# Kernel optimization log

Hardware: AMD Instinct MI355X
Metric: run time of the kernel (lower is better)

## Reference

```python
import jax, jax.numpy as jnp
import numpy as np

N, F_DIM, H_DIM = 8192, 128, 128

def setup_inputs() -> dict:
    key = jax.random.key(0)
    ks = jax.random.split(key, 7)
    inp = {
        "input": jax.random.normal(ks[0], (N, F_DIM), dtype=jnp.float32),
        "wavelets": jax.random.normal(ks[1], (N, N), dtype=jnp.float32) / np.sqrt(N),
        "wavelets_inv": jax.random.normal(ks[2], (N, N), dtype=jnp.float32) / np.sqrt(N),
        # layer 1 params
        "W1": jax.random.uniform(ks[3], (F_DIM, H_DIM), dtype=jnp.float32,
                                 minval=-np.sqrt(6.0/(F_DIM+H_DIM)), maxval=np.sqrt(6.0/(F_DIM+H_DIM))),
        "f1": jax.random.uniform(ks[4], (N,), dtype=jnp.float32, minval=0.9, maxval=1.1),
        # layer 2 params
        "W2": jax.random.uniform(ks[5], (H_DIM, H_DIM), dtype=jnp.float32,
                                 minval=-np.sqrt(6.0/(H_DIM+H_DIM)), maxval=np.sqrt(6.0/(H_DIM+H_DIM))),
        "f2": jax.random.uniform(ks[6], (N,), dtype=jnp.float32, minval=0.9, maxval=1.1),
    }
    return inp

def _gwnn_layer(features, wavelets, wavelets_inv, W, filt):
    # torch: wavelets @ diag(filt) @ (wavelets_inv @ (features @ W))
    # diag(filt) matmul == column-wise scale of wavelets (broadcast elementwise)
    xw = features @ W                      # [N, out]
    spec = wavelets_inv @ xw               # [N, out] spectral-domain features
    spec = filt[:, None] * spec            # apply learnable diagonal filter
    return wavelets @ spec                 # [N, out]

def reference(input, wavelets, wavelets_inv, W1, f1, W2, f2):
    # eval mode: dropout is identity
    h1 = jax.nn.relu(_gwnn_layer(input, wavelets, wavelets_inv, W1, f1))
    out = _gwnn_layer(h1, wavelets, wavelets_inv, W2, f2)
    return out
```

## Files before the change

kernel.cpp:

```cpp
#include <hip/hip_runtime.h>
#include <hip/hip_bf16.h>
#include <stdint.h>


typedef __attribute__((ext_vector_type(4))) float f32x4;
typedef __attribute__((ext_vector_type(8))) short s16x8;
typedef __attribute__((ext_vector_type(4))) short s16x4;

#define DEVI static __device__ __forceinline__

DEVI short bf1(float x){ __bf16 h = (__bf16)x; return __builtin_bit_cast(short, h); }

DEVI s16x8 cvt8(f32x4 lo, f32x4 hi){
  s16x8 r;
#pragma unroll
  for (int i = 0; i < 4; ++i){ r[i] = bf1(lo[i]); r[4+i] = bf1(hi[i]); }
  return r;
}

DEVI void glds16(const void* g, void* l){
  __builtin_amdgcn_global_load_lds((const __attribute__((address_space(1))) void*)g,
                                   (__attribute__((address_space(3))) void*)l, 16, 0, 0);
}

template<int N> DEVI void waitvm(){
  if constexpr (N == 0)       asm volatile("s_waitcnt vmcnt(0)"  ::: "memory");
  else if constexpr (N == 5)  asm volatile("s_waitcnt vmcnt(5)"  ::: "memory");
  else if constexpr (N == 6)  asm volatile("s_waitcnt vmcnt(6)"  ::: "memory");
  else if constexpr (N == 10) asm volatile("s_waitcnt vmcnt(10)" ::: "memory");
  else if constexpr (N == 12) asm volatile("s_waitcnt vmcnt(12)" ::: "memory");
  else if constexpr (N == 15) asm volatile("s_waitcnt vmcnt(15)" ::: "memory");
  else if constexpr (N == 18) asm volatile("s_waitcnt vmcnt(18)" ::: "memory");
  else if constexpr (N == 20) asm volatile("s_waitcnt vmcnt(20)" ::: "memory");
  else if constexpr (N == 24) asm volatile("s_waitcnt vmcnt(24)" ::: "memory");
}

template<bool ABF, bool SCALE, bool RELU, int OUTM>
__global__ __launch_bounds__(256, 1) void gemm_k(
    const void* __restrict__ Ap, const short* __restrict__ Btp,
    const float* __restrict__ fp, void* __restrict__ Outp, int K, int M)
{
  constexpr int BM = 32, BN = 128, BK = 64;
  constexpr int ASZ = ABF ? BM*BK*2 : BM*BK*4;
  constexpr int BSZ = BN*BK*2;
  constexpr int TSZ = ASZ + BSZ;
  constexpr int NL  = ABF ? 5 : 6;
  constexpr int NBUF = 6;
  constexpr int PRE  = 5;
  __shared__ uint8_t lds[NBUF*TSZ];

  const int tid  = threadIdx.x;
  const int lane = tid & 63;
  const int wv   = tid >> 6;
  const int la   = lane & 15;
  const int g4   = lane >> 4;
  const int m0   = blockIdx.x * BM;

  const float* gA0 = nullptr; const float* gA1 = nullptr; const short* gAh = nullptr;
  if constexpr (!ABF){
    const float* Af = (const float*)Ap;
    int r0 = (wv<<3) + (lane>>4);
    int r1 = r0 + 4;
    gA0 = Af + (size_t)(m0+r0)*K + (((lane&15)^(r0&15))<<2);
    gA1 = Af + (size_t)(m0+r1)*K + (((lane&15)^(r1&15))<<2);
  } else {
    const short* Ah = (const short*)Ap;
    int r = (wv<<3) + (lane>>3);
    gAh = Ah + (size_t)(m0+r)*K + (((lane&7)^(r&7))<<3);
  }
  const int nb0 = (wv<<5) + (lane>>3);
  const short* gB0 = Btp + (size_t)(nb0    )*K + (((lane&7)^(nb0&7))<<3);
  const short* gB1 = Btp + (size_t)(nb0+ 8 )*K + (((lane&7)^(nb0&7))<<3);
  const short* gB2 = Btp + (size_t)(nb0+16 )*K + (((lane&7)^(nb0&7))<<3);
  const short* gB3 = Btp + (size_t)(nb0+24 )*K + (((lane&7)^(nb0&7))<<3);

  int aoff[2][2][2];
  int boff[2][2];
#pragma unroll
  for (int mi = 0; mi < 2; ++mi){
    const int r = mi*16 + la;
#pragma unroll
    for (int kf = 0; kf < 2; ++kf){
      if constexpr (!ABF){
        const int v0 = kf*8 + (g4<<1);
        aoff[mi][kf][0] = r*256 + (((v0  )^(r&15))<<4);
        aoff[mi][kf][1] = r*256 + (((v0+1)^(r&15))<<4);
      } else {
        const int u = kf*4 + g4;
        aoff[mi][kf][0] = r*128 + ((u^(r&7))<<4);
        aoff[mi][kf][1] = 0;
      }
    }
  }
#pragma unroll
  for (int ni = 0; ni < 2; ++ni){
    const int n = (wv<<5) + ni*16 + la;
#pragma unroll
    for (int kf = 0; kf < 2; ++kf){
      const int u = kf*4 + g4;
      boff[ni][kf] = n*128 + ((u^(n&7))<<4);
    }
  }

  f32x4 acc[2][2] = {};

  auto STAGE = [&](uint8_t* buf){
    uint8_t* Ab = buf;
    uint8_t* Bb = buf + ASZ;
    if constexpr (!ABF){
      glds16(gA0, Ab + (wv<<11));
      glds16(gA1, Ab + (wv<<11) + 1024);
      gA0 += BK; gA1 += BK;
    } else {
      glds16(gAh, Ab + (wv<<10));
      gAh += BK;
    }
    glds16(gB0, Bb + (wv<<12));
    glds16(gB1, Bb + (wv<<12) + 1024);
    glds16(gB2, Bb + (wv<<12) + 2048);
    glds16(gB3, Bb + (wv<<12) + 3072);
    gB0 += BK; gB1 += BK; gB2 += BK; gB3 += BK;
  };

  auto COMPUTE = [&](const uint8_t* buf){
    const uint8_t* Ab = buf;
    const uint8_t* Bb = buf + ASZ;
#pragma unroll
    for (int kf = 0; kf < 2; ++kf){
      s16x8 a0, a1, b0, b1;
      if constexpr (!ABF){
        a0 = cvt8(*(const f32x4*)(Ab + aoff[0][kf][0]), *(const f32x4*)(Ab + aoff[0][kf][1]));
        a1 = cvt8(*(const f32x4*)(Ab + aoff[1][kf][0]), *(const f32x4*)(Ab + aoff[1][kf][1]));
      } else {
        a0 = *(const s16x8*)(Ab + aoff[0][kf][0]);
        a1 = *(const s16x8*)(Ab + aoff[1][kf][0]);
      }
      b0 = *(const s16x8*)(Bb + boff[0][kf]);
      b1 = *(const s16x8*)(Bb + boff[1][kf]);
      acc[0][0] = __builtin_amdgcn_mfma_f32_16x16x32_bf16(a0, b0, acc[0][0], 0, 0, 0);
      acc[0][1] = __builtin_amdgcn_mfma_f32_16x16x32_bf16(a0, b1, acc[0][1], 0, 0, 0);
      acc[1][0] = __builtin_amdgcn_mfma_f32_16x16x32_bf16(a1, b0, acc[1][0], 0, 0, 0);
      acc[1][1] = __builtin_amdgcn_mfma_f32_16x16x32_bf16(a1, b1, acc[1][1], 0, 0, 0);
    }
  };

  const int nsteps = K >> 6;

  uint8_t* const lend = lds + NBUF*TSZ;
  uint8_t* bs = lds;
  uint8_t* bc = lds;

  for (int s = 0; s < PRE && s < nsteps; ++s){
    STAGE(bs);
    bs += TSZ; if (bs == lend) bs = lds;
  }

  for (int t = 0; t < nsteps; ++t){
    const int ahead = nsteps - 1 - t;
    if (ahead >= 4)      waitvm<4*NL>();
    else if (ahead == 3) waitvm<3*NL>();
    else if (ahead == 2) waitvm<2*NL>();
    else if (ahead == 1) waitvm<1*NL>();
    else                 waitvm<0>();
    __builtin_amdgcn_s_barrier();
    asm volatile("" ::: "memory");
    if (t + PRE < nsteps){
      STAGE(bs);
      bs += TSZ; if (bs == lend) bs = lds;
    }
    COMPUTE(bc);
    bc += TSZ; if (bc == lend) bc = lds;
    asm volatile("" ::: "memory");
  }

  const int mbase = m0 + (g4<<2);
  const int nc0   = (wv<<5) + la;
  f32x4 fv0, fv1;
  if constexpr (SCALE){
    fv0 = *(const f32x4*)(fp + mbase);
    fv1 = *(const f32x4*)(fp + mbase + 16);
  }
#pragma unroll
  for (int mi = 0; mi < 2; ++mi){
#pragma unroll
    for (int ni = 0; ni < 2; ++ni){
      f32x4 v = acc[mi][ni];
      if constexpr (SCALE) v = v * (mi ? fv1 : fv0);
      if constexpr (RELU){
#pragma unroll
        for (int r = 0; r < 4; ++r) v[r] = fmaxf(v[r], 0.0f);
      }
      if constexpr (OUTM == 2){
        s16x4 pk;
#pragma unroll
        for (int r = 0; r < 4; ++r) pk[r] = bf1(v[r]);
        *(s16x4*)((short*)Outp + (size_t)(nc0 + (ni<<4))*M + (mbase + (mi<<4))) = pk;
      } else if constexpr (OUTM == 1){
#pragma unroll
        for (int r = 0; r < 4; ++r)
          ((short*)Outp)[(size_t)(mbase + (mi<<4) + r)*BN + nc0 + (ni<<4)] = bf1(v[r]);
      } else {
#pragma unroll
        for (int r = 0; r < 4; ++r)
          ((float*)Outp)[(size_t)(mbase + (mi<<4) + r)*BN + nc0 + (ni<<4)] = v[r];
      }
    }
  }
}

__global__ void wtrans_k(const float* __restrict__ W1, const float* __restrict__ W2,
                         short* __restrict__ T1, short* __restrict__ T2){
  const int idx = blockIdx.x*256 + threadIdx.x;
  const int m = idx >> 14, rem = idx & 16383;
  const int n = rem >> 7, k = rem & 127;
  const float* W = m ? W2 : W1;
  short* T = m ? T2 : T1;
  T[n*128 + k] = bf1(W[k*128 + n]);
}

extern "C" void kernel_launch(void* const* d_in, const int* in_sizes, int n_in,
                              void* d_out, int out_size, void* d_ws, size_t ws_size,
                              hipStream_t stream){
  const float* input = (const float*)d_in[0];
  const float* wav   = (const float*)d_in[1];
  const float* winv  = (const float*)d_in[2];
  const float* W1    = (const float*)d_in[3];
  const float* f1    = (const float*)d_in[4];
  const float* W2    = (const float*)d_in[5];
  const float* f2    = (const float*)d_in[6];

  uint8_t* ws = (uint8_t*)d_ws;
  short* W1T = (short*)(ws);
  short* W2T = (short*)(ws + (32<<10));
  short* XWT = (short*)(ws + (64<<10));
  short* SPT = (short*)(ws + (64<<10) + (2<<20));
  short* H1  = (short*)(ws + (64<<10) + (4<<20));

  constexpr int M = 8192;
  dim3 b(256), g(M/32), gt(128);

  wtrans_k<<<gt, b, 0, stream>>>(W1, W2, W1T, W2T);
  gemm_k<false,false,false,2><<<g,b,0,stream>>>(input, W1T, nullptr, XWT, 128, M);
  gemm_k<false,true ,false,2><<<g,b,0,stream>>>(winv,  XWT, f1,      SPT, M,   M);
  gemm_k<false,false,true ,1><<<g,b,0,stream>>>(wav,   SPT, nullptr, H1,  M,   M);
  gemm_k<true ,false,false,2><<<g,b,0,stream>>>(H1,    W2T, nullptr, XWT, 128, M);
  gemm_k<false,true ,false,2><<<g,b,0,stream>>>(winv,  XWT, f2,      SPT, M,   M);
  gemm_k<false,false,false,0><<<g,b,0,stream>>>(wav,   SPT, nullptr, d_out, M, M);
}
```

Measured before the change: 326.8 us.

## Split K across two wave groups per block and reduce partials in LDS

```diff
diff --git a/kernel.cpp b/kernel.cpp
--- a/kernel.cpp
+++ b/kernel.cpp
@@ -24,19 +24,13 @@
 }
 
 template<int N> DEVI void waitvm(){
-  if constexpr (N == 0)       asm volatile("s_waitcnt vmcnt(0)"  ::: "memory");
-  else if constexpr (N == 5)  asm volatile("s_waitcnt vmcnt(5)"  ::: "memory");
-  else if constexpr (N == 6)  asm volatile("s_waitcnt vmcnt(6)"  ::: "memory");
-  else if constexpr (N == 10) asm volatile("s_waitcnt vmcnt(10)" ::: "memory");
-  else if constexpr (N == 12) asm volatile("s_waitcnt vmcnt(12)" ::: "memory");
-  else if constexpr (N == 15) asm volatile("s_waitcnt vmcnt(15)" ::: "memory");
-  else if constexpr (N == 18) asm volatile("s_waitcnt vmcnt(18)" ::: "memory");
-  else if constexpr (N == 20) asm volatile("s_waitcnt vmcnt(20)" ::: "memory");
-  else if constexpr (N == 24) asm volatile("s_waitcnt vmcnt(24)" ::: "memory");
+  if constexpr (N == 0)      asm volatile("s_waitcnt vmcnt(0)" ::: "memory");
+  else if constexpr (N == 5) asm volatile("s_waitcnt vmcnt(5)" ::: "memory");
+  else if constexpr (N == 6) asm volatile("s_waitcnt vmcnt(6)" ::: "memory");
 }
 
 template<bool ABF, bool SCALE, bool RELU, int OUTM>
-__global__ __launch_bounds__(256, 1) void gemm_k(
+__global__ __launch_bounds__(512, 1) void gemm_k(
     const void* __restrict__ Ap, const short* __restrict__ Btp,
     const float* __restrict__ fp, void* __restrict__ Outp, int K, int M)
 {
@@ -45,34 +39,39 @@
   constexpr int BSZ = BN*BK*2;
   constexpr int TSZ = ASZ + BSZ;
   constexpr int NL  = ABF ? 5 : 6;
-  constexpr int NBUF = 6;
-  constexpr int PRE  = 5;
-  __shared__ uint8_t lds[NBUF*TSZ];
+  constexpr int NBUF = 3;
+  constexpr int PRE  = 2;
+  __shared__ uint8_t lds[2*NBUF*TSZ];
 
   const int tid  = threadIdx.x;
   const int lane = tid & 63;
   const int wv   = tid >> 6;
+  const int kh   = wv >> 2;
+  const int w4   = wv & 3;
   const int la   = lane & 15;
   const int g4   = lane >> 4;
   const int m0   = blockIdx.x * BM;
+  const int K2   = K >> 1;
+  const size_t kb = (size_t)kh * K2;
+  uint8_t* const hl = lds + kh*(NBUF*TSZ);
 
   const float* gA0 = nullptr; const float* gA1 = nullptr; const short* gAh = nullptr;
   if constexpr (!ABF){
     const float* Af = (const float*)Ap;
-    int r0 = (wv<<3) + (lane>>4);
+    int r0 = (w4<<3) + (lane>>4);
     int r1 = r0 + 4;
-    gA0 = Af + (size_t)(m0+r0)*K + (((lane&15)^(r0&15))<<2);
-    gA1 = Af + (size_t)(m0+r1)*K + (((lane&15)^(r1&15))<<2);
+    gA0 = Af + (size_t)(m0+r0)*K + kb + (((lane&15)^(r0&15))<<2);
+    gA1 = Af + (size_t)(m0+r1)*K + kb + (((lane&15)^(r1&15))<<2);
   } else {
     const short* Ah = (const short*)Ap;
-    int r = (wv<<3) + (lane>>3);
-    gAh = Ah + (size_t)(m0+r)*K + (((lane&7)^(r&7))<<3);
-  }
-  const int nb0 = (wv<<5) + (lane>>3);
-  const short* gB0 = Btp + (size_t)(nb0    )*K + (((lane&7)^(nb0&7))<<3);
-  const short* gB1 = Btp + (size_t)(nb0+ 8 )*K + (((lane&7)^(nb0&7))<<3);
-  const short* gB2 = Btp + (size_t)(nb0+16 )*K + (((lane&7)^(nb0&7))<<3);
-  const short* gB3 = Btp + (size_t)(nb0+24 )*K + (((lane&7)^(nb0&7))<<3);
+    int r = (w4<<3) + (lane>>3);
+    gAh = Ah + (size_t)(m0+r)*K + kb + (((lane&7)^(r&7))<<3);
+  }
+  const int nb0 = (w4<<5) + (lane>>3);
+  const short* gB0 = Btp + (size_t)(nb0    )*K + kb + (((lane&7)^(nb0&7))<<3);
+  const short* gB1 = Btp + (size_t)(nb0+ 8 )*K + kb + (((lane&7)^(nb0&7))<<3);
+  const short* gB2 = Btp + (size_t)(nb0+16 )*K + kb + (((lane&7)^(nb0&7))<<3);
+  const short* gB3 = Btp + (size_t)(nb0+24 )*K + kb + (((lane&7)^(nb0&7))<<3);
 
   int aoff[2][2][2];
   int boff[2][2];
@@ -94,7 +93,7 @@
   }
 #pragma unroll
   for (int ni = 0; ni < 2; ++ni){
-    const int n = (wv<<5) + ni*16 + la;
+    const int n = (w4<<5) + ni*16 + la;
 #pragma unroll
     for (int kf = 0; kf < 2; ++kf){
       const int u = kf*4 + g4;
@@ -108,17 +107,17 @@
     uint8_t* Ab = buf;
     uint8_t* Bb = buf + ASZ;
     if constexpr (!ABF){
-      glds16(gA0, Ab + (wv<<11));
-      glds16(gA1, Ab + (wv<<11) + 1024);
+      glds16(gA0, Ab + (w4<<11));
+      glds16(gA1, Ab + (w4<<11) + 1024);
       gA0 += BK; gA1 += BK;
     } else {
-      glds16(gAh, Ab + (wv<<10));
+      glds16(gAh, Ab + (w4<<10));
       gAh += BK;
     }
-    glds16(gB0, Bb + (wv<<12));
-    glds16(gB1, Bb + (wv<<12) + 1024);
-    glds16(gB2, Bb + (wv<<12) + 2048);
-    glds16(gB3, Bb + (wv<<12) + 3072);
+    glds16(gB0, Bb + (w4<<12));
+    glds16(gB1, Bb + (w4<<12) + 1024);
+    glds16(gB2, Bb + (w4<<12) + 2048);
+    glds16(gB3, Bb + (w4<<12) + 3072);
     gB0 += BK; gB1 += BK; gB2 += BK; gB3 += BK;
   };
 
@@ -144,37 +143,56 @@
     }
   };
 
-  const int nsteps = K >> 6;
-
-  uint8_t* const lend = lds + NBUF*TSZ;
-  uint8_t* bs = lds;
-  uint8_t* bc = lds;
+  const int nsteps = K2 >> 6;
+
+  uint8_t* const lend = hl + NBUF*TSZ;
+  uint8_t* bs = hl;
+  uint8_t* bc = hl;
 
   for (int s = 0; s < PRE && s < nsteps; ++s){
     STAGE(bs);
-    bs += TSZ; if (bs == lend) bs = lds;
+    bs += TSZ; if (bs == lend) bs = hl;
   }
 
   for (int t = 0; t < nsteps; ++t){
-    const int ahead = nsteps - 1 - t;
-    if (ahead >= 4)      waitvm<4*NL>();
-    else if (ahead == 3) waitvm<3*NL>();
-    else if (ahead == 2) waitvm<2*NL>();
-    else if (ahead == 1) waitvm<1*NL>();
-    else                 waitvm<0>();
+    if (t < nsteps - 1) waitvm<NL>();
+    else                waitvm<0>();
     __builtin_amdgcn_s_barrier();
     asm volatile("" ::: "memory");
     if (t + PRE < nsteps){
       STAGE(bs);
-      bs += TSZ; if (bs == lend) bs = lds;
+      bs += TSZ; if (bs == lend) bs = hl;
     }
     COMPUTE(bc);
-    bc += TSZ; if (bc == lend) bc = lds;
+    bc += TSZ; if (bc == lend) bc = hl;
     asm volatile("" ::: "memory");
   }
 
+  __builtin_amdgcn_s_barrier();
+  float* red = (float*)lds;
+  const int rbase = (w4<<6) + lane;
+  if (kh == 1){
+#pragma unroll
+    for (int mi = 0; mi < 2; ++mi)
+#pragma unroll
+      for (int ni = 0; ni < 2; ++ni)
+#pragma unroll
+        for (int r = 0; r < 4; ++r)
+          red[((((mi<<1)+ni)<<2 | r) << 8) + rbase] = acc[mi][ni][r];
+  }
+  asm volatile("s_waitcnt lgkmcnt(0)" ::: "memory");
+  __builtin_amdgcn_s_barrier();
+  if (kh == 1) return;
+#pragma unroll
+  for (int mi = 0; mi < 2; ++mi)
+#pragma unroll
+    for (int ni = 0; ni < 2; ++ni)
+#pragma unroll
+      for (int r = 0; r < 4; ++r)
+        acc[mi][ni][r] += red[((((mi<<1)+ni)<<2 | r) << 8) + rbase];
+
   const int mbase = m0 + (g4<<2);
-  const int nc0   = (wv<<5) + la;
+  const int nc0   = (w4<<5) + la;
   f32x4 fv0, fv1;
   if constexpr (SCALE){
     fv0 = *(const f32x4*)(fp + mbase);
@@ -237,9 +255,9 @@
   short* H1  = (short*)(ws + (64<<10) + (4<<20));
 
   constexpr int M = 8192;
-  dim3 b(256), g(M/32), gt(128);
-
-  wtrans_k<<<gt, b, 0, stream>>>(W1, W2, W1T, W2T);
+  dim3 b(512), g(M/32), gt(128), bt(256);
+
+  wtrans_k<<<gt, bt, 0, stream>>>(W1, W2, W1T, W2T);
   gemm_k<false,false,false,2><<<g,b,0,stream>>>(input, W1T, nullptr, XWT, 128, M);
   gemm_k<false,true ,false,2><<<g,b,0,stream>>>(winv,  XWT, f1,      SPT, M,   M);
   gemm_k<false,false,true ,1><<<g,b,0,stream>>>(wav,   SPT, nullptr, H1,  M,   M);
```

New measurement: 318.0 us. -2.7%, faster.

## Split-K the large NxN GEMMs in two with separate reduction epilogue kernels

Applied to the files above, without the earlier changes.

```diff
diff --git a/kernel.cpp b/kernel.cpp
--- a/kernel.cpp
+++ b/kernel.cpp
@@ -24,29 +24,142 @@
 }
 
 template<int N> DEVI void waitvm(){
-  if constexpr (N == 0)       asm volatile("s_waitcnt vmcnt(0)"  ::: "memory");
-  else if constexpr (N == 5)  asm volatile("s_waitcnt vmcnt(5)"  ::: "memory");
-  else if constexpr (N == 6)  asm volatile("s_waitcnt vmcnt(6)"  ::: "memory");
-  else if constexpr (N == 10) asm volatile("s_waitcnt vmcnt(10)" ::: "memory");
-  else if constexpr (N == 12) asm volatile("s_waitcnt vmcnt(12)" ::: "memory");
-  else if constexpr (N == 15) asm volatile("s_waitcnt vmcnt(15)" ::: "memory");
-  else if constexpr (N == 18) asm volatile("s_waitcnt vmcnt(18)" ::: "memory");
-  else if constexpr (N == 20) asm volatile("s_waitcnt vmcnt(20)" ::: "memory");
-  else if constexpr (N == 24) asm volatile("s_waitcnt vmcnt(24)" ::: "memory");
-}
-
-template<bool ABF, bool SCALE, bool RELU, int OUTM>
+  if constexpr (N == 0)      asm volatile("s_waitcnt vmcnt(0)" ::: "memory");
+  else if constexpr (N == 5) asm volatile("s_waitcnt vmcnt(5)" ::: "memory");
+  else if constexpr (N == 6) asm volatile("s_waitcnt vmcnt(6)" ::: "memory");
+}
+
+__global__ __launch_bounds__(256, 2) void gemm_sk(
+    const float* __restrict__ Ap, const short* __restrict__ Btp,
+    float* __restrict__ Pp, int K, int M)
+{
+  constexpr int BM = 32, BN = 128, BK = 64;
+  constexpr int ASZ = BM*BK*4;
+  constexpr int BSZ = BN*BK*2;
+  constexpr int TSZ = ASZ + BSZ;
+  constexpr int NL  = 6;
+  constexpr int NBUF = 3, PRE = 2;
+  __shared__ uint8_t lds[NBUF*TSZ];
+
+  const int tid  = threadIdx.x;
+  const int lane = tid & 63;
+  const int wv   = tid >> 6;
+  const int la   = lane & 15;
+  const int g4   = lane >> 4;
+  const int m0   = blockIdx.x * BM;
+  const int kh   = blockIdx.y;
+  const int K2   = K >> 1;
+  const size_t kb = (size_t)kh * K2;
+
+  const float* Af = Ap;
+  int r0 = (wv<<3) + (lane>>4);
+  int r1 = r0 + 4;
+  const float* gA0 = Af + (size_t)(m0+r0)*K + kb + (((lane&15)^(r0&15))<<2);
+  const float* gA1 = Af + (size_t)(m0+r1)*K + kb + (((lane&15)^(r1&15))<<2);
+  const int nb0 = (wv<<5) + (lane>>3);
+  const short* gB0 = Btp + (size_t)(nb0    )*K + kb + (((lane&7)^(nb0&7))<<3);
+  const short* gB1 = Btp + (size_t)(nb0+ 8 )*K + kb + (((lane&7)^(nb0&7))<<3);
+  const short* gB2 = Btp + (size_t)(nb0+16 )*K + kb + (((lane&7)^(nb0&7))<<3);
+  const short* gB3 = Btp + (size_t)(nb0+24 )*K + kb + (((lane&7)^(nb0&7))<<3);
+
+  int aoff[2][2][2];
+  int boff[2][2];
+#pragma unroll
+  for (int mi = 0; mi < 2; ++mi){
+    const int r = mi*16 + la;
+#pragma unroll
+    for (int kf = 0; kf < 2; ++kf){
+      const int v0 = kf*8 + (g4<<1);
+      aoff[mi][kf][0] = r*256 + (((v0  )^(r&15))<<4);
+      aoff[mi][kf][1] = r*256 + (((v0+1)^(r&15))<<4);
+    }
+  }
+#pragma unroll
+  for (int ni = 0; ni < 2; ++ni){
+    const int n = (wv<<5) + ni*16 + la;
+#pragma unroll
+    for (int kf = 0; kf < 2; ++kf){
+      const int u = kf*4 + g4;
+      boff[ni][kf] = n*128 + ((u^(n&7))<<4);
+    }
+  }
+
+  f32x4 acc[2][2] = {};
+
+  auto STAGE = [&](uint8_t* buf){
+    uint8_t* Ab = buf;
+    uint8_t* Bb = buf + ASZ;
+    glds16(gA0, Ab + (wv<<11));
+    glds16(gA1, Ab + (wv<<11) + 1024);
+    gA0 += BK; gA1 += BK;
+    glds16(gB0, Bb + (wv<<12));
+    glds16(gB1, Bb + (wv<<12) + 1024);
+    glds16(gB2, Bb + (wv<<12) + 2048);
+    glds16(gB3, Bb + (wv<<12) + 3072);
+    gB0 += BK; gB1 += BK; gB2 += BK; gB3 += BK;
+  };
+
+  auto COMPUTE = [&](const uint8_t* buf){
+    const uint8_t* Ab = buf;
+    const uint8_t* Bb = buf + ASZ;
+#pragma unroll
+    for (int kf = 0; kf < 2; ++kf){
+      s16x8 a0 = cvt8(*(const f32x4*)(Ab + aoff[0][kf][0]), *(const f32x4*)(Ab + aoff[0][kf][1]));
+      s16x8 a1 = cvt8(*(const f32x4*)(Ab + aoff[1][kf][0]), *(const f32x4*)(Ab + aoff[1][kf][1]));
+      s16x8 b0 = *(const s16x8*)(Bb + boff[0][kf]);
+      s16x8 b1 = *(const s16x8*)(Bb + boff[1][kf]);
+      acc[0][0] = __builtin_amdgcn_mfma_f32_16x16x32_bf16(a0, b0, acc[0][0], 0, 0, 0);
+      acc[0][1] = __builtin_amdgcn_mfma_f32_16x16x32_bf16(a0, b1, acc[0][1], 0, 0, 0);
+      acc[1][0] = __builtin_amdgcn_mfma_f32_16x16x32_bf16(a1, b0, acc[1][0], 0, 0, 0);
+      acc[1][1] = __builtin_amdgcn_mfma_f32_16x16x32_bf16(a1, b1, acc[1][1], 0, 0, 0);
+    }
+  };
+
+  const int nsteps = K2 >> 6;
+  uint8_t* const lend = lds + NBUF*TSZ;
+  uint8_t* bs = lds;
+  uint8_t* bc = lds;
+  for (int s = 0; s < PRE && s < nsteps; ++s){
+    STAGE(bs);
+    bs += TSZ; if (bs == lend) bs = lds;
+  }
+  for (int t = 0; t < nsteps; ++t){
+    if (t < nsteps - 1) waitvm<NL>();
+    else                waitvm<0>();
+    __builtin_amdgcn_s_barrier();
+    asm volatile("" ::: "memory");
+    if (t + PRE < nsteps){
+      STAGE(bs);
+      bs += TSZ; if (bs == lend) bs = lds;
+    }
+    COMPUTE(bc);
+    bc += TSZ; if (bc == lend) bc = lds;
+    asm volatile("" ::: "memory");
+  }
+
+  float* P = Pp + (size_t)kh * M * 128;
+  const int mbase = m0 + (g4<<2);
+  const int nc0   = (wv<<5) + la;
+#pragma unroll
+  for (int mi = 0; mi < 2; ++mi)
+#pragma unroll
+    for (int ni = 0; ni < 2; ++ni)
+#pragma unroll
+      for (int r = 0; r < 4; ++r)
+        P[(size_t)(mbase + (mi<<4) + r)*128 + nc0 + (ni<<4)] = acc[mi][ni][r];
+}
+
+template<bool ABF>
 __global__ __launch_bounds__(256, 1) void gemm_k(
     const void* __restrict__ Ap, const short* __restrict__ Btp,
-    const float* __restrict__ fp, void* __restrict__ Outp, int K, int M)
+    void* __restrict__ Outp, int K, int M)
 {
   constexpr int BM = 32, BN = 128, BK = 64;
   constexpr int ASZ = ABF ? BM*BK*2 : BM*BK*4;
   constexpr int BSZ = BN*BK*2;
   constexpr int TSZ = ASZ + BSZ;
   constexpr int NL  = ABF ? 5 : 6;
-  constexpr int NBUF = 6;
-  constexpr int PRE  = 5;
+  constexpr int NBUF = 3, PRE = 2;
   __shared__ uint8_t lds[NBUF*TSZ];
 
   const int tid  = threadIdx.x;
@@ -145,23 +258,16 @@
   };
 
   const int nsteps = K >> 6;
-
   uint8_t* const lend = lds + NBUF*TSZ;
   uint8_t* bs = lds;
   uint8_t* bc = lds;
-
   for (int s = 0; s < PRE && s < nsteps; ++s){
     STAGE(bs);
     bs += TSZ; if (bs == lend) bs = lds;
   }
-
   for (int t = 0; t < nsteps; ++t){
-    const int ahead = nsteps - 1 - t;
-    if (ahead >= 4)      waitvm<4*NL>();
-    else if (ahead == 3) waitvm<3*NL>();
-    else if (ahead == 2) waitvm<2*NL>();
-    else if (ahead == 1) waitvm<1*NL>();
-    else                 waitvm<0>();
+    if (t < nsteps - 1) waitvm<NL>();
+    else                waitvm<0>();
     __builtin_amdgcn_s_barrier();
     asm volatile("" ::: "memory");
     if (t + PRE < nsteps){
@@ -175,37 +281,77 @@
 
   const int mbase = m0 + (g4<<2);
   const int nc0   = (wv<<5) + la;
-  f32x4 fv0, fv1;
-  if constexpr (SCALE){
-    fv0 = *(const f32x4*)(fp + mbase);
-    fv1 = *(const f32x4*)(fp + mbase + 16);
-  }
 #pragma unroll
   for (int mi = 0; mi < 2; ++mi){
 #pragma unroll
     for (int ni = 0; ni < 2; ++ni){
-      f32x4 v = acc[mi][ni];
-      if constexpr (SCALE) v = v * (mi ? fv1 : fv0);
-      if constexpr (RELU){
-#pragma unroll
-        for (int r = 0; r < 4; ++r) v[r] = fmaxf(v[r], 0.0f);
-      }
-      if constexpr (OUTM == 2){
-        s16x4 pk;
-#pragma unroll
-        for (int r = 0; r < 4; ++r) pk[r] = bf1(v[r]);
-        *(s16x4*)((short*)Outp + (size_t)(nc0 + (ni<<4))*M + (mbase + (mi<<4))) = pk;
-      } else if constexpr (OUTM == 1){
-#pragma unroll
-        for (int r = 0; r < 4; ++r)
-          ((short*)Outp)[(size_t)(mbase + (mi<<4) + r)*BN + nc0 + (ni<<4)] = bf1(v[r]);
-      } else {
-#pragma unroll
-        for (int r = 0; r < 4; ++r)
-          ((float*)Outp)[(size_t)(mbase + (mi<<4) + r)*BN + nc0 + (ni<<4)] = v[r];
-      }
-    }
-  }
+      s16x4 pk;
+#pragma unroll
+      for (int r = 0; r < 4; ++r) pk[r] = bf1(acc[mi][ni][r]);
+      *(s16x4*)((short*)Outp + (size_t)(nc0 + (ni<<4))*M + (mbase + (mi<<4))) = pk;
+    }
+  }
+}
+
+
+__global__ __launch_bounds__(256) void red_t(
+    const float* __restrict__ Pp, const float* __restrict__ fp,
+    short* __restrict__ out, int M)
+{
+  __shared__ short t[128*65];
+  const float* P0 = Pp;
+  const float* P1 = Pp + (size_t)M*128;
+  const int m0 = blockIdx.x * 64;
+  const int tid = threadIdx.x;
+#pragma unroll
+  for (int it = 0; it < 8; ++it){
+    const int idx = it*256 + tid;
+    const int m = idx >> 5, nq = idx & 31;
+    f32x4 a = ((const f32x4*)(P0 + (size_t)(m0+m)*128))[nq];
+    f32x4 b = ((const f32x4*)(P1 + (size_t)(m0+m)*128))[nq];
+    const float fv = fp[m0+m];
+#pragma unroll
+    for (int j = 0; j < 4; ++j)
+      t[(nq*4+j)*65 + m] = bf1(fv * (a[j] + b[j]));
+  }
+  __syncthreads();
+#pragma unroll
+  for (int it = 0; it < 8; ++it){
+    const int idx = it*256 + tid;
+    const int n = idx >> 4, mc = idx & 15;
+    s16x4 v;
+#pragma unroll
+    for (int j = 0; j < 4; ++j) v[j] = t[n*65 + mc*4 + j];
+    *(s16x4*)(out + (size_t)n*M + m0 + mc*4) = v;
+  }
+}
+
+__global__ __launch_bounds__(256) void red_r(
+    const float* __restrict__ Pp, short* __restrict__ out, int M)
+{
+  const float* P0 = Pp;
+  const float* P1 = Pp + (size_t)M*128;
+  const size_t i0 = (size_t)(blockIdx.x*256 + threadIdx.x) * 8;
+  f32x4 a0 = ((const f32x4*)(P0 + i0))[0], a1 = ((const f32x4*)(P0 + i0))[1];
+  f32x4 b0 = ((const f32x4*)(P1 + i0))[0], b1 = ((const f32x4*)(P1 + i0))[1];
+  s16x8 v;
+#pragma unroll
+  for (int j = 0; j < 4; ++j){
+    v[j]   = bf1(fmaxf(a0[j] + b0[j], 0.0f));
+    v[4+j] = bf1(fmaxf(a1[j] + b1[j], 0.0f));
+  }
+  *(s16x8*)(out + i0) = v;
+}
+
+__global__ __launch_bounds__(256) void red_f(
+    const float* __restrict__ Pp, float* __restrict__ out, int M)
+{
+  const float* P0 = Pp;
+  const float* P1 = Pp + (size_t)M*128;
+  const size_t i0 = (size_t)(blockIdx.x*256 + threadIdx.x) * 4;
+  f32x4 a = *(const f32x4*)(P0 + i0);
+  f32x4 b = *(const f32x4*)(P1 + i0);
+  *(f32x4*)(out + i0) = a + b;
 }
 
 __global__ void wtrans_k(const float* __restrict__ W1, const float* __restrict__ W2,
@@ -235,15 +381,26 @@
   short* XWT = (short*)(ws + (64<<10));
   short* SPT = (short*)(ws + (64<<10) + (2<<20));
   short* H1  = (short*)(ws + (64<<10) + (4<<20));
+  float* P   = (float*)(ws + (64<<10) + (6<<20));
 
   constexpr int M = 8192;
-  dim3 b(256), g(M/32), gt(128);
+  dim3 b(256);
+  dim3 gsk(M/32, 2);
+  dim3 gns(M/32);
+  dim3 grt(M/64);
+  dim3 grr(M*128/(256*8));
+  dim3 grf(M*128/(256*4));
+  dim3 gt(128);
 
   wtrans_k<<<gt, b, 0, stream>>>(W1, W2, W1T, W2T);
-  gemm_k<false,false,false,2><<<g,b,0,stream>>>(input, W1T, nullptr, XWT, 128, M);
-  gemm_k<false,true ,false,2><<<g,b,0,stream>>>(winv,  XWT, f1,      SPT, M,   M);
-  gemm_k<false,false,true ,1><<<g,b,0,stream>>>(wav,   SPT, nullptr, H1,  M,   M);
-  gemm_k<true ,false,false,2><<<g,b,0,stream>>>(H1,    W2T, nullptr, XWT, 128, M);
-  gemm_k<false,true ,false,2><<<g,b,0,stream>>>(winv,  XWT, f2,      SPT, M,   M);
-  gemm_k<false,false,false,0><<<g,b,0,stream>>>(wav,   SPT, nullptr, d_out, M, M);
-}
+  gemm_k<false><<<gns, b, 0, stream>>>(input, W1T, XWT, 128, M);
+  gemm_sk<<<gsk, b, 0, stream>>>(winv, XWT, P, M, M);
+  red_t  <<<grt, b, 0, stream>>>(P, f1, SPT, M);
+  gemm_sk<<<gsk, b, 0, stream>>>(wav, SPT, P, M, M);
+  red_r  <<<grr, b, 0, stream>>>(P, H1, M);
+  gemm_k<true ><<<gns, b, 0, stream>>>(H1, W2T, XWT, 128, M);
+  gemm_sk<<<gsk, b, 0, stream>>>(winv, XWT, P, M, M);
+  red_t  <<<grt, b, 0, stream>>>(P, f2, SPT, M);
+  gemm_sk<<<gsk, b, 0, stream>>>(wav, SPT, P, M, M);
+  red_f  <<<grf, b, 0, stream>>>(P, (float*)d_out, M);
+}
```

Measured after the change: 346.9 us. +6.1%, slower.

## Add register-fed B GEMM with smaller M tile and two blocks per CU for big GEMMs

Applied to the files above, without the earlier changes.

```diff
diff --git a/kernel.cpp b/kernel.cpp
--- a/kernel.cpp
+++ b/kernel.cpp
@@ -24,29 +24,143 @@
 }
 
 template<int N> DEVI void waitvm(){
-  if constexpr (N == 0)       asm volatile("s_waitcnt vmcnt(0)"  ::: "memory");
-  else if constexpr (N == 5)  asm volatile("s_waitcnt vmcnt(5)"  ::: "memory");
-  else if constexpr (N == 6)  asm volatile("s_waitcnt vmcnt(6)"  ::: "memory");
-  else if constexpr (N == 10) asm volatile("s_waitcnt vmcnt(10)" ::: "memory");
-  else if constexpr (N == 12) asm volatile("s_waitcnt vmcnt(12)" ::: "memory");
-  else if constexpr (N == 15) asm volatile("s_waitcnt vmcnt(15)" ::: "memory");
-  else if constexpr (N == 18) asm volatile("s_waitcnt vmcnt(18)" ::: "memory");
-  else if constexpr (N == 20) asm volatile("s_waitcnt vmcnt(20)" ::: "memory");
-  else if constexpr (N == 24) asm volatile("s_waitcnt vmcnt(24)" ::: "memory");
-}
-
-template<bool ABF, bool SCALE, bool RELU, int OUTM>
+  if constexpr (N == 0)      asm volatile("s_waitcnt vmcnt(0)" ::: "memory");
+  else if constexpr (N == 4) asm volatile("s_waitcnt vmcnt(4)" ::: "memory");
+  else if constexpr (N == 5) asm volatile("s_waitcnt vmcnt(5)" ::: "memory");
+  else if constexpr (N == 6) asm volatile("s_waitcnt vmcnt(6)" ::: "memory");
+}
+
+template<bool SCALE, bool RELU, int OUTM>
+__global__ __launch_bounds__(256, 2) void gemm_bd(
+    const float* __restrict__ Ap, const short* __restrict__ Btp,
+    const float* __restrict__ fp, void* __restrict__ Outp, int K, int M)
+{
+  constexpr int BM = 16, BK = 64;
+  constexpr int ASZ = BM*BK*4;
+  constexpr int NBUF = 6;
+  __shared__ uint8_t lds[NBUF*ASZ];
+
+  const int tid  = threadIdx.x;
+  const int lane = tid & 63;
+  const int wv   = tid >> 6;
+  const int la   = lane & 15;
+  const int g4   = lane >> 4;
+  const int m0   = blockIdx.x * BM;
+
+  const int rA = (wv<<2) + g4;
+  const float* gA = Ap + (size_t)(m0+rA)*K + ((la ^ rA)<<2);
+
+  int aoff[2][2];
+#pragma unroll
+  for (int kf = 0; kf < 2; ++kf){
+    const int v0 = kf*8 + (g4<<1);
+    aoff[kf][0] = la*256 + (((v0  )^la)<<4);
+    aoff[kf][1] = la*256 + (((v0+1)^la)<<4);
+  }
+
+  const int n0 = (wv<<5) + la;
+  const short* gBn0 = Btp + (size_t)(n0   )*K + (g4<<3);
+  const short* gBn1 = Btp + (size_t)(n0+16)*K + (g4<<3);
+
+  f32x4 acc[2] = {};
+  s16x8 Be[4], Bo[4];
+
+  uint8_t* const lend = lds + NBUF*ASZ;
+  uint8_t* bs = lds;
+  uint8_t* bc = lds;
+
+  auto STAGE = [&](){
+    glds16(gA, bs + (wv<<10));
+    gA += BK;
+    bs += ASZ; if (bs == lend) bs = lds;
+  };
+  auto LOADB = [&](s16x8* B, int t1){
+    const short* p0 = gBn0 + (size_t)t1*BK;
+    const short* p1 = gBn1 + (size_t)t1*BK;
+    B[0] = *(const s16x8*)(p0);
+    B[1] = *(const s16x8*)(p0 + 32);
+    B[2] = *(const s16x8*)(p1);
+    B[3] = *(const s16x8*)(p1 + 32);
+  };
+  auto COMPUTE = [&](const s16x8* B){
+    const uint8_t* buf = bc;
+#pragma unroll
+    for (int kf = 0; kf < 2; ++kf){
+      s16x8 a = cvt8(*(const f32x4*)(buf + aoff[kf][0]),
+                     *(const f32x4*)(buf + aoff[kf][1]));
+      acc[0] = __builtin_amdgcn_mfma_f32_16x16x32_bf16(a, B[kf],   acc[0], 0, 0, 0);
+      acc[1] = __builtin_amdgcn_mfma_f32_16x16x32_bf16(a, B[2+kf], acc[1], 0, 0, 0);
+    }
+    bc += ASZ; if (bc == lend) bc = lds;
+  };
+
+  const int ns = K >> 6;
+
+  STAGE(); STAGE(); STAGE(); STAGE();
+  LOADB(Be, 0);
+
+  for (int t = 0; t < ns; t += 2){
+    LOADB(Bo, t+1);
+    if (t + 4 < ns) STAGE();
+    if (t == 0 || t == ns-4) waitvm<5>();
+    else if (t == ns-2)      waitvm<4>();
+    else                     waitvm<6>();
+    __builtin_amdgcn_s_barrier();
+    asm volatile("" ::: "memory");
+    COMPUTE(Be);
+    asm volatile("" ::: "memory");
+    const int u = t + 1;
+    if (u + 1 < ns) LOADB(Be, u+1);
+    if (u + 4 < ns) STAGE();
+    if (u == ns-3)      waitvm<4>();
+    else if (u == ns-1) waitvm<0>();
+    else                waitvm<6>();
+    __builtin_amdgcn_s_barrier();
+    asm volatile("" ::: "memory");
+    COMPUTE(Bo);
+    asm volatile("" ::: "memory");
+  }
+
+  const int mbase = m0 + (g4<<2);
+  const int nc0   = (wv<<5) + la;
+  f32x4 fv;
+  if constexpr (SCALE) fv = *(const f32x4*)(fp + mbase);
+#pragma unroll
+  for (int ni = 0; ni < 2; ++ni){
+    f32x4 v = acc[ni];
+    if constexpr (SCALE) v = v * fv;
+    if constexpr (RELU){
+#pragma unroll
+      for (int r = 0; r < 4; ++r) v[r] = fmaxf(v[r], 0.0f);
+    }
+    if constexpr (OUTM == 2){
+      s16x4 pk;
+#pragma unroll
+      for (int r = 0; r < 4; ++r) pk[r] = bf1(v[r]);
+      *(s16x4*)((short*)Outp + (size_t)(nc0 + (ni<<4))*M + mbase) = pk;
+    } else if constexpr (OUTM == 1){
+#pragma unroll
+      for (int r = 0; r < 4; ++r)
+        ((short*)Outp)[(size_t)(mbase + r)*128 + nc0 + (ni<<4)] = bf1(v[r]);
+    } else {
+#pragma unroll
+      for (int r = 0; r < 4; ++r)
+        ((float*)Outp)[(size_t)(mbase + r)*128 + nc0 + (ni<<4)] = v[r];
+    }
+  }
+}
+
+template<bool ABF>
 __global__ __launch_bounds__(256, 1) void gemm_k(
     const void* __restrict__ Ap, const short* __restrict__ Btp,
-    const float* __restrict__ fp, void* __restrict__ Outp, int K, int M)
+    void* __restrict__ Outp, int K, int M)
 {
   constexpr int BM = 32, BN = 128, BK = 64;
   constexpr int ASZ = ABF ? BM*BK*2 : BM*BK*4;
   constexpr int BSZ = BN*BK*2;
   constexpr int TSZ = ASZ + BSZ;
   constexpr int NL  = ABF ? 5 : 6;
-  constexpr int NBUF = 6;
-  constexpr int PRE  = 5;
+  constexpr int NBUF = 3, PRE = 2;
   __shared__ uint8_t lds[NBUF*TSZ];
 
   const int tid  = threadIdx.x;
@@ -145,23 +259,16 @@
   };
 
   const int nsteps = K >> 6;
-
   uint8_t* const lend = lds + NBUF*TSZ;
   uint8_t* bs = lds;
   uint8_t* bc = lds;
-
   for (int s = 0; s < PRE && s < nsteps; ++s){
     STAGE(bs);
     bs += TSZ; if (bs == lend) bs = lds;
   }
-
   for (int t = 0; t < nsteps; ++t){
-    const int ahead = nsteps - 1 - t;
-    if (ahead >= 4)      waitvm<4*NL>();
-    else if (ahead == 3) waitvm<3*NL>();
-    else if (ahead == 2) waitvm<2*NL>();
-    else if (ahead == 1) waitvm<1*NL>();
-    else                 waitvm<0>();
+    if (t < nsteps - 1) waitvm<NL>();
+    else                waitvm<0>();
     __builtin_amdgcn_s_barrier();
     asm volatile("" ::: "memory");
     if (t + PRE < nsteps){
@@ -175,35 +282,14 @@
 
   const int mbase = m0 + (g4<<2);
   const int nc0   = (wv<<5) + la;
-  f32x4 fv0, fv1;
-  if constexpr (SCALE){
-    fv0 = *(const f32x4*)(fp + mbase);
-    fv1 = *(const f32x4*)(fp + mbase + 16);
-  }
 #pragma unroll
   for (int mi = 0; mi < 2; ++mi){
 #pragma unroll
     for (int ni = 0; ni < 2; ++ni){
-      f32x4 v = acc[mi][ni];
-      if constexpr (SCALE) v = v * (mi ? fv1 : fv0);
-      if constexpr (RELU){
-#pragma unroll
-        for (int r = 0; r < 4; ++r) v[r] = fmaxf(v[r], 0.0f);
-      }
-      if constexpr (OUTM == 2){
-        s16x4 pk;
-#pragma unroll
-        for (int r = 0; r < 4; ++r) pk[r] = bf1(v[r]);
-        *(s16x4*)((short*)Outp + (size_t)(nc0 + (ni<<4))*M + (mbase + (mi<<4))) = pk;
-      } else if constexpr (OUTM == 1){
-#pragma unroll
-        for (int r = 0; r < 4; ++r)
-          ((short*)Outp)[(size_t)(mbase + (mi<<4) + r)*BN + nc0 + (ni<<4)] = bf1(v[r]);
-      } else {
-#pragma unroll
-        for (int r = 0; r < 4; ++r)
-          ((float*)Outp)[(size_t)(mbase + (mi<<4) + r)*BN + nc0 + (ni<<4)] = v[r];
-      }
+      s16x4 pk;
+#pragma unroll
+      for (int r = 0; r < 4; ++r) pk[r] = bf1(acc[mi][ni][r]);
+      *(s16x4*)((short*)Outp + (size_t)(nc0 + (ni<<4))*M + (mbase + (mi<<4))) = pk;
     }
   }
 }
@@ -237,13 +323,16 @@
   short* H1  = (short*)(ws + (64<<10) + (4<<20));
 
   constexpr int M = 8192;
-  dim3 b(256), g(M/32), gt(128);
+  dim3 b(256);
+  dim3 gbd(M/16);
+  dim3 gns(M/32);
+  dim3 gt(128);
 
   wtrans_k<<<gt, b, 0, stream>>>(W1, W2, W1T, W2T);
-  gemm_k<false,false,false,2><<<g,b,0,stream>>>(input, W1T, nullptr, XWT, 128, M);
-  gemm_k<false,true ,false,2><<<g,b,0,stream>>>(winv,  XWT, f1,      SPT, M,   M);
-  gemm_k<false,false,true ,1><<<g,b,0,stream>>>(wav,   SPT, nullptr, H1,  M,   M);
-  gemm_k<true ,false,false,2><<<g,b,0,stream>>>(H1,    W2T, nullptr, XWT, 128, M);
-  gemm_k<false,true ,false,2><<<g,b,0,stream>>>(winv,  XWT, f2,      SPT, M,   M);
-  gemm_k<false,false,false,0><<<g,b,0,stream>>>(wav,   SPT, nullptr, d_out, M, M);
-}
+  gemm_k<false><<<gns, b, 0, stream>>>(input, W1T, XWT, 128, M);
+  gemm_bd<true ,false,2><<<gbd, b, 0, stream>>>(winv, XWT, f1, SPT, M, M);
+  gemm_bd<false,true ,1><<<gbd, b, 0, stream>>>(wav,  SPT, nullptr, H1, M, M);
+  gemm_k<true ><<<gns, b, 0, stream>>>(H1, W2T, XWT, 128, M);
+  gemm_bd<true ,false,2><<<gbd, b, 0, stream>>>(winv, XWT, f2, SPT, M, M);
+  gemm_bd<false,false,0><<<gbd, b, 0, stream>>>(wav,  SPT, nullptr, d_out, M, M);
+}
```

Measured after the change: 529.0 us. 61.9% more time.
